# Performance work log

Hardware: AMD Instinct MI355X
Metric: run time of the kernel (lower is better)

## Reference

```python
import jax, jax.numpy as jnp
import numpy as np

B = 524288
D = 128  # z_dim

def setup_inputs() -> dict:
    key = jax.random.key(0)
    kx, ky = jax.random.split(key)
    x = jax.random.normal(kx, (B, D), dtype=jnp.float32)
    y = jax.random.normal(ky, (B, D), dtype=jnp.float32)
    return {"x": x, "y": y}

def reference(x, y):
    # IQE-style quasimetric distance (QuasiMetric.get_distance)
    d = x.shape[-1]
    valid = x < y                                  # [B, D] bool
    xy = jnp.concatenate([x, y], axis=-1)          # [B, 2D]
    ixy = jnp.argsort(xy, axis=-1)                 # [B, 2D] indices
    sxy = jnp.take_along_axis(xy, ixy, axis=-1)    # sorted values
    sign = jnp.where(ixy < d, -1, 1)               # -1 for x entries, +1 for y
    neg_inc = jnp.take_along_axis(valid, ixy % d, axis=-1).astype(jnp.int32) * sign
    neg_cum = jnp.cumsum(neg_inc, axis=-1)
    neg_f = jnp.where(neg_cum < 0, -1.0, 0.0).astype(sxy.dtype)
    neg_incf = jnp.concatenate([neg_f[..., :1], jnp.diff(neg_f, axis=-1)], axis=-1)
    return (sxy * neg_incf).sum(-1)                # [B]
```

## Files before the change

### kernel.cpp

```cpp
#include <hip/hip_runtime.h>
#include <float.h>


constexpr int D = 128;
#define INF __builtin_huge_valf()

__device__ inline float med3(float a, float b, float c) {
    return __builtin_amdgcn_fmed3f(a, b, c);
}

template<int M>
__device__ inline float swzx(float v) {
    int i = __builtin_amdgcn_ds_swizzle(__float_as_int(v), (M << 10) | 0x1F);
    return __int_as_float(i);
}

__device__ inline void cea(float& u, float& v) { float lo = fminf(u, v), hi = fmaxf(u, v); u = lo; v = hi; }
__device__ inline void ced(float& u, float& v) { float lo = fminf(u, v), hi = fmaxf(u, v); u = hi; v = lo; }
__device__ inline void cek(float& u, float& v, float s) {
    float lo = med3(u, v, s), hi = med3(u, v, -s); u = lo; v = hi;
}

template<int M>
__device__ inline void cross2(float (&a)[8], float (&b)[8], float sel) {
    float ta[8], tb[8];
    #pragma unroll
    for (int r = 0; r < 8; r++) { ta[r] = swzx<M>(a[r]); tb[r] = swzx<M>(b[r]); }
    #pragma unroll
    for (int r = 0; r < 8; r++) { a[r] = med3(a[r], ta[r], sel); b[r] = med3(b[r], tb[r], sel); }
}

__device__ inline void inlane3x2(float (&a)[8], float (&b)[8], float s) {
    cek(a[0],a[4],s); cek(a[1],a[5],s); cek(a[2],a[6],s); cek(a[3],a[7],s);
    cek(b[0],b[4],s); cek(b[1],b[5],s); cek(b[2],b[6],s); cek(b[3],b[7],s);
    cek(a[0],a[2],s); cek(a[1],a[3],s); cek(a[4],a[6],s); cek(a[5],a[7],s);
    cek(b[0],b[2],s); cek(b[1],b[3],s); cek(b[4],b[6],s); cek(b[5],b[7],s);
    cek(a[0],a[1],s); cek(a[2],a[3],s); cek(a[4],a[5],s); cek(a[6],a[7],s);
    cek(b[0],b[1],s); cek(b[2],b[3],s); cek(b[4],b[5],s); cek(b[6],b[7],s);
}

__global__ __launch_bounds__(256) void iqe_union_kernel(
    const float* __restrict__ x, const float* __restrict__ y,
    float* __restrict__ out, int B)
{
    const int tid = threadIdx.x;
    const int g   = tid & 15;
    const int row = blockIdx.x * 16 + (tid >> 4);
    if (row >= B) return;

    const size_t base = (size_t)row * D + g * 8;
    float xs[8], ys[8];
    *reinterpret_cast<float4*>(&xs[0]) = *reinterpret_cast<const float4*>(x + base);
    *reinterpret_cast<float4*>(&xs[4]) = *reinterpret_cast<const float4*>(x + base + 4);
    *reinterpret_cast<float4*>(&ys[0]) = *reinterpret_cast<const float4*>(y + base);
    *reinterpret_cast<float4*>(&ys[4]) = *reinterpret_cast<const float4*>(y + base + 4);

    float a[8], b[8];
    #pragma unroll
    for (int r = 0; r < 8; r++) {
        const bool v = xs[r] < ys[r];
        a[r] = v ? xs[r] : FLT_MAX;
        b[r] = v ? ys[r] : FLT_MAX;
    }

    const float S1 = (g & 1) ? 1.f : -1.f;
    const float S2 = (g & 2) ? 1.f : -1.f;
    const float S4 = (g & 4) ? 1.f : -1.f;
    const float S8 = (g & 8) ? 1.f : -1.f;
    const float M1 = S1 * INF, M2 = S2 * INF, M4 = S4 * INF, M8 = S8 * INF;
    const float N2 = -M2, N4 = -M4, N8 = -M8;

    cea(a[0],a[1]); ced(a[2],a[3]); cea(a[4],a[5]); ced(a[6],a[7]);
    cea(b[0],b[1]); ced(b[2],b[3]); cea(b[4],b[5]); ced(b[6],b[7]);
    cea(a[0],a[2]); cea(a[1],a[3]); ced(a[4],a[6]); ced(a[5],a[7]);
    cea(b[0],b[2]); cea(b[1],b[3]); ced(b[4],b[6]); ced(b[5],b[7]);
    cea(a[0],a[1]); cea(a[2],a[3]); ced(a[4],a[5]); ced(a[6],a[7]);
    cea(b[0],b[1]); cea(b[2],b[3]); ced(b[4],b[5]); ced(b[6],b[7]);
    inlane3x2(a, b, M1);
    cross2<1>(a, b, S1 * N2);
    inlane3x2(a, b, M2);
    cross2<2>(a, b, S2 * N4);
    cross2<1>(a, b, S1 * N4);
    inlane3x2(a, b, M4);
    cross2<4>(a, b, S4 * N8);
    cross2<2>(a, b, S2 * N8);
    cross2<1>(a, b, S1 * N8);
    inlane3x2(a, b, M8);
    cross2<8>(a, b, M8);
    cross2<4>(a, b, M4);
    cross2<2>(a, b, M2);
    cross2<1>(a, b, M1);
    cea(a[0],a[4]); cea(a[1],a[5]); cea(a[2],a[6]); cea(a[3],a[7]);
    cea(b[0],b[4]); cea(b[1],b[5]); cea(b[2],b[6]); cea(b[3],b[7]);
    cea(a[0],a[2]); cea(a[1],a[3]); cea(a[4],a[6]); cea(a[5],a[7]);
    cea(b[0],b[2]); cea(b[1],b[3]); cea(b[4],b[6]); cea(b[5],b[7]);
    cea(a[0],a[1]); cea(a[2],a[3]); cea(a[4],a[5]); cea(a[6],a[7]);
    cea(b[0],b[1]); cea(b[2],b[3]); cea(b[4],b[5]); cea(b[6],b[7]);

    float prev = __shfl_up(b[7], 1, 64);
    if (g == 0) prev = -FLT_MAX;
    float c = 0.f;
    #pragma unroll
    for (int r = 0; r < 8; r++) {
        c += fmaxf(0.f, b[r] - fmaxf(a[r], prev));
        prev = b[r];
    }
    c += swzx<1>(c); c += swzx<2>(c); c += swzx<4>(c); c += swzx<8>(c);
    if (g == 0) out[row] = c;
}

extern "C" void kernel_launch(void* const* d_in, const int* in_sizes, int n_in,
                              void* d_out, int out_size, void* d_ws, size_t ws_size,
                              hipStream_t stream) {
    const float* x = (const float*)d_in[0];
    const float* y = (const float*)d_in[1];
    float* out = (float*)d_out;
    const int B = in_sizes[0] / D;
    const int blocks = (B + 15) / 16;
    iqe_union_kernel<<<blocks, 256, 0, stream>>>(x, y, out, B);
}
```

Before: 521.8 us.

## Sort 32 elements per lane with 4 lanes per row using DPP crosses

Each row is now handled by 4 lanes holding 32 elements each instead of 16 lanes holding 8, so most bitonic merge stages become in-register compare-exchanges. The few remaining cross-lane stages use quad-permute DPP moves instead of ds_swizzle, which avoids LDS-path latency. The cost is much higher register pressure (64+ floats per lane), which may lower occupancy, and the loads become strided float4 accesses interleaved across the four lanes.

```diff
diff --git a/kernel.cpp b/kernel.cpp
--- a/kernel.cpp
+++ b/kernel.cpp
@@ -9,11 +9,14 @@
     return __builtin_amdgcn_fmed3f(a, b, c);
 }
 
-template<int M>
-__device__ inline float swzx(float v) {
-    int i = __builtin_amdgcn_ds_swizzle(__float_as_int(v), (M << 10) | 0x1F);
+template<int CTRL>
+__device__ inline float dppmov(float v) {
+    int i = __builtin_amdgcn_mov_dpp(__float_as_int(v), CTRL, 0xF, 0xF, true);
     return __int_as_float(i);
 }
+constexpr int QP_XOR1 = 0xB1;
+constexpr int QP_XOR2 = 0x4E;
+constexpr int QP_SHR1 = 0x90;
 
 __device__ inline void cea(float& u, float& v) { float lo = fminf(u, v), hi = fmaxf(u, v); u = lo; v = hi; }
 __device__ inline void ced(float& u, float& v) { float lo = fminf(u, v), hi = fmaxf(u, v); u = hi; v = lo; }
@@ -21,22 +24,25 @@
     float lo = med3(u, v, s), hi = med3(u, v, -s); u = lo; v = hi;
 }
 
-template<int M>
-__device__ inline void cross2(float (&a)[8], float (&b)[8], float sel) {
-    float ta[8], tb[8];
+template<int K, int J>
+__device__ inline void sub_ct(float (&v)[32]) {
     #pragma unroll
-    for (int r = 0; r < 8; r++) { ta[r] = swzx<M>(a[r]); tb[r] = swzx<M>(b[r]); }
+    for (int r = 0; r < 32; r++)
+        if (!(r & J)) { if (!(r & K)) cea(v[r], v[r + J]); else ced(v[r], v[r + J]); }
+}
+template<int J>
+__device__ inline void sub_rt(float (&v)[32], float s) {
     #pragma unroll
-    for (int r = 0; r < 8; r++) { a[r] = med3(a[r], ta[r], sel); b[r] = med3(b[r], tb[r], sel); }
+    for (int r = 0; r < 32; r++)
+        if (!(r & J)) cek(v[r], v[r + J], s);
 }
-
-__device__ inline void inlane3x2(float (&a)[8], float (&b)[8], float s) {
-    cek(a[0],a[4],s); cek(a[1],a[5],s); cek(a[2],a[6],s); cek(a[3],a[7],s);
-    cek(b[0],b[4],s); cek(b[1],b[5],s); cek(b[2],b[6],s); cek(b[3],b[7],s);
-    cek(a[0],a[2],s); cek(a[1],a[3],s); cek(a[4],a[6],s); cek(a[5],a[7],s);
-    cek(b[0],b[2],s); cek(b[1],b[3],s); cek(b[4],b[6],s); cek(b[5],b[7],s);
-    cek(a[0],a[1],s); cek(a[2],a[3],s); cek(a[4],a[5],s); cek(a[6],a[7],s);
-    cek(b[0],b[1],s); cek(b[2],b[3],s); cek(b[4],b[5],s); cek(b[6],b[7],s);
+template<int CTRL>
+__device__ inline void cross(float (&v)[32], float sel) {
+    #pragma unroll
+    for (int r = 0; r < 32; r++) {
+        float t = dppmov<CTRL>(v[r]);
+        v[r] = med3(v[r], t, sel);
+    }
 }
 
 __global__ __launch_bounds__(256) void iqe_union_kernel(
@@ -44,68 +50,69 @@
     float* __restrict__ out, int B)
 {
     const int tid = threadIdx.x;
-    const int g   = tid & 15;
-    const int row = blockIdx.x * 16 + (tid >> 4);
+    const int g   = tid & 3;
+    const int row = blockIdx.x * 64 + (tid >> 2);
     if (row >= B) return;
 
-    const size_t base = (size_t)row * D + g * 8;
-    float xs[8], ys[8];
-    *reinterpret_cast<float4*>(&xs[0]) = *reinterpret_cast<const float4*>(x + base);
-    *reinterpret_cast<float4*>(&xs[4]) = *reinterpret_cast<const float4*>(x + base + 4);
-    *reinterpret_cast<float4*>(&ys[0]) = *reinterpret_cast<const float4*>(y + base);
-    *reinterpret_cast<float4*>(&ys[4]) = *reinterpret_cast<const float4*>(y + base + 4);
-
-    float a[8], b[8];
+    const size_t rbase = (size_t)row * D;
+    float a[32], b[32];
     #pragma unroll
-    for (int r = 0; r < 8; r++) {
-        const bool v = xs[r] < ys[r];
-        a[r] = v ? xs[r] : FLT_MAX;
-        b[r] = v ? ys[r] : FLT_MAX;
+    for (int t = 0; t < 8; t++) {
+        *reinterpret_cast<float4*>(&a[4 * t]) = *reinterpret_cast<const float4*>(x + rbase + 16 * t + 4 * g);
+        *reinterpret_cast<float4*>(&b[4 * t]) = *reinterpret_cast<const float4*>(y + rbase + 16 * t + 4 * g);
+    }
+    #pragma unroll
+    for (int r = 0; r < 32; r++) {
+        const bool v = a[r] < b[r];
+        a[r] = v ? a[r] : FLT_MAX;
+        b[r] = v ? b[r] : FLT_MAX;
     }
 
     const float S1 = (g & 1) ? 1.f : -1.f;
     const float S2 = (g & 2) ? 1.f : -1.f;
-    const float S4 = (g & 4) ? 1.f : -1.f;
-    const float S8 = (g & 8) ? 1.f : -1.f;
-    const float M1 = S1 * INF, M2 = S2 * INF, M4 = S4 * INF, M8 = S8 * INF;
-    const float N2 = -M2, N4 = -M4, N8 = -M8;
+    const float M1 = S1 * INF;
+    const float M2 = S2 * INF;
+    const float C1 = -S1 * S2 * INF;
 
-    cea(a[0],a[1]); ced(a[2],a[3]); cea(a[4],a[5]); ced(a[6],a[7]);
-    cea(b[0],b[1]); ced(b[2],b[3]); cea(b[4],b[5]); ced(b[6],b[7]);
-    cea(a[0],a[2]); cea(a[1],a[3]); ced(a[4],a[6]); ced(a[5],a[7]);
-    cea(b[0],b[2]); cea(b[1],b[3]); ced(b[4],b[6]); ced(b[5],b[7]);
-    cea(a[0],a[1]); cea(a[2],a[3]); ced(a[4],a[5]); ced(a[6],a[7]);
-    cea(b[0],b[1]); cea(b[2],b[3]); ced(b[4],b[5]); ced(b[6],b[7]);
-    inlane3x2(a, b, M1);
-    cross2<1>(a, b, S1 * N2);
-    inlane3x2(a, b, M2);
-    cross2<2>(a, b, S2 * N4);
-    cross2<1>(a, b, S1 * N4);
-    inlane3x2(a, b, M4);
-    cross2<4>(a, b, S4 * N8);
-    cross2<2>(a, b, S2 * N8);
-    cross2<1>(a, b, S1 * N8);
-    inlane3x2(a, b, M8);
-    cross2<8>(a, b, M8);
-    cross2<4>(a, b, M4);
-    cross2<2>(a, b, M2);
-    cross2<1>(a, b, M1);
-    cea(a[0],a[4]); cea(a[1],a[5]); cea(a[2],a[6]); cea(a[3],a[7]);
-    cea(b[0],b[4]); cea(b[1],b[5]); cea(b[2],b[6]); cea(b[3],b[7]);
-    cea(a[0],a[2]); cea(a[1],a[3]); cea(a[4],a[6]); cea(a[5],a[7]);
-    cea(b[0],b[2]); cea(b[1],b[3]); cea(b[4],b[6]); cea(b[5],b[7]);
-    cea(a[0],a[1]); cea(a[2],a[3]); cea(a[4],a[5]); cea(a[6],a[7]);
-    cea(b[0],b[1]); cea(b[2],b[3]); cea(b[4],b[5]); cea(b[6],b[7]);
+    sub_ct<2, 1>(a);  sub_ct<2, 1>(b);
+    sub_ct<4, 2>(a);  sub_ct<4, 2>(b);
+    sub_ct<4, 1>(a);  sub_ct<4, 1>(b);
+    sub_ct<8, 4>(a);  sub_ct<8, 4>(b);
+    sub_ct<8, 2>(a);  sub_ct<8, 2>(b);
+    sub_ct<8, 1>(a);  sub_ct<8, 1>(b);
+    sub_ct<16, 8>(a); sub_ct<16, 8>(b);
+    sub_ct<16, 4>(a); sub_ct<16, 4>(b);
+    sub_ct<16, 2>(a); sub_ct<16, 2>(b);
+    sub_ct<16, 1>(a); sub_ct<16, 1>(b);
+    sub_rt<16>(a, M1); sub_rt<16>(b, M1);
+    sub_rt<8>(a, M1);  sub_rt<8>(b, M1);
+    sub_rt<4>(a, M1);  sub_rt<4>(b, M1);
+    sub_rt<2>(a, M1);  sub_rt<2>(b, M1);
+    sub_rt<1>(a, M1);  sub_rt<1>(b, M1);
+    cross<QP_XOR1>(a, C1); cross<QP_XOR1>(b, C1);
+    sub_rt<16>(a, M2); sub_rt<16>(b, M2);
+    sub_rt<8>(a, M2);  sub_rt<8>(b, M2);
+    sub_rt<4>(a, M2);  sub_rt<4>(b, M2);
+    sub_rt<2>(a, M2);  sub_rt<2>(b, M2);
+    sub_rt<1>(a, M2);  sub_rt<1>(b, M2);
+    cross<QP_XOR2>(a, M2); cross<QP_XOR2>(b, M2);
+    cross<QP_XOR1>(a, M1); cross<QP_XOR1>(b, M1);
+    sub_ct<128, 16>(a); sub_ct<128, 16>(b);
+    sub_ct<128, 8>(a);  sub_ct<128, 8>(b);
+    sub_ct<128, 4>(a);  sub_ct<128, 4>(b);
+    sub_ct<128, 2>(a);  sub_ct<128, 2>(b);
+    sub_ct<128, 1>(a);  sub_ct<128, 1>(b);
 
-    float prev = __shfl_up(b[7], 1, 64);
+    float prev = dppmov<QP_SHR1>(b[31]);
     if (g == 0) prev = -FLT_MAX;
     float c = 0.f;
     #pragma unroll
-    for (int r = 0; r < 8; r++) {
+    for (int r = 0; r < 32; r++) {
         c += fmaxf(0.f, b[r] - fmaxf(a[r], prev));
         prev = b[r];
     }
-    c += swzx<1>(c); c += swzx<2>(c); c += swzx<4>(c); c += swzx<8>(c);
+    c += dppmov<QP_XOR1>(c);
+    c += dppmov<QP_XOR2>(c);
     if (g == 0) out[row] = c;
 }
 
@@ -116,6 +123,6 @@
     const float* y = (const float*)d_in[1];
     float* out = (float*)d_out;
     const int B = in_sizes[0] / D;
-    const int blocks = (B + 15) / 16;
+    const int blocks = (B + 63) / 64;
     iqe_union_kernel<<<blocks, 256, 0, stream>>>(x, y, out, B);
 }
```

Measured after the change: 523.8 us. About the same (+0.4%).
